# Performance work log

Hardware: AMD Instinct MI355X
Metric: run time of the kernel (lower is better)

The kernel has to match this reference:

```python
import jax, jax.numpy as jnp
import numpy as np

N, E = 30000, 240000          # nodes, edges per view
IN, D, OUT = 512, 128, 64      # in_dim, hidden_dim, out_dim
V, BLK, H, DM = 2, 2, 2, 64    # num_view, blk_size, num_heads, gate max-pool dim
NEG_ATT, NEG_OUT = 0.2, 0.01   # leaky_relu slopes (attention / outer)


def setup_inputs() -> dict:
    key = jax.random.key(0)
    ks = jax.random.split(key, 12)
    s = 0.05
    f32 = jnp.float32
    return {
        "ft": jax.random.normal(ks[0], (N, IN), f32),
        "src": jax.random.randint(ks[1], (V, E), 0, N, jnp.int32),
        "dst": jax.random.randint(ks[2], (V, E), 0, N, jnp.int32),
        "W_proj": jax.random.normal(ks[3], (IN, D), f32) * s,
        "W_embed": jax.random.normal(ks[4], (D, D), f32) * s,
        "a_l": jax.random.normal(ks[5], (V, BLK, H, D), f32) * s,
        "a_r": jax.random.normal(ks[6], (V, BLK, H, D), f32) * s,
        "Wv": jax.random.normal(ks[7], (V, BLK, H, D, D), f32) * s,
        "Wgm": jax.random.normal(ks[8], (V, BLK, D, DM), f32) * s,
        "Wgate": jax.random.normal(ks[9], (V, BLK, 2 * D + DM, H), f32) * s,
        "b_gate": jnp.zeros((V, BLK, H), f32),
        "W_tran": jax.random.normal(ks[10], (2 * D + DM and (D + V * H * D), OUT), f32) * s if False else jax.random.normal(ks[10], (D + V * H * D, OUT), f32) * s,
        "b_tran": jnp.zeros((OUT,), f32),
    }


def _seg_sum(x, idx):
    return jax.ops.segment_sum(x, idx, num_segments=N)


def _cgaan_layer(v, z, s_idx, d_idx, al, ar, wv, wgm, wgate, bg, merge):
    # v: [N,D] values, z: [N,D] attention features ('proj_z')
    # Multi-head attention logits: e_ij = leaky_relu(a_l.z_src + a_r.z_dst)  [E,H]
    logit_l = jnp.einsum("nd,hd->nh", z, al)
    logit_r = jnp.einsum("nd,hd->nh", z, ar)
    e = jax.nn.leaky_relu(logit_l[s_idx] + logit_r[d_idx], NEG_ATT)
    # edge softmax over incoming edges of each dst node
    m = jax.ops.segment_max(e, d_idx, num_segments=N)          # [N,H]
    ex = jnp.exp(e - m[d_idx])
    denom = _seg_sum(ex, d_idx)                                 # [N,H]
    alpha = ex / denom[d_idx]                                   # [E,H]
    # per-head value projection and weighted aggregation
    wvn = jnp.einsum("nd,hde->nhe", v, wv)                      # [N,H,D]
    agg = _seg_sum(alpha[:, :, None] * wvn[s_idx], d_idx)       # [N,H,D]
    # GaAN-style gate: sigmoid(FC([x_i, mean_j v_j, max_j (v_j Wgm)])) -> per-head scalar
    deg = _seg_sum(jnp.ones((s_idx.shape[0],), v.dtype), d_idx)  # [N]
    mean_n = _seg_sum(v[s_idx], d_idx) / jnp.maximum(deg, 1.0)[:, None]
    mx = jax.ops.segment_max((v @ wgm)[s_idx], d_idx, num_segments=N)
    mx = jnp.where(deg[:, None] > 0, mx, 0.0)                   # isolated nodes -> 0
    g = jax.nn.sigmoid(jnp.concatenate([v, mean_n, mx], -1) @ wgate + bg)  # [N,H]
    agg = g[:, :, None] * agg
    if merge == "mean":
        return agg.mean(axis=1)                                 # [N,D]
    return agg.reshape(agg.shape[0], -1)                        # cat -> [N,H*D]


def reference(ft, src, dst, W_proj, W_embed, a_l, a_r, Wv, Wgm, Wgate, b_gate, W_tran, b_tran):
    proj = ft @ W_proj                                          # [N,D]
    cur = [proj for _ in range(V)]
    for i in range(BLK):
        merge = "mean" if i < BLK - 1 else "cat"
        nxt = []
        for j in range(V):
            z = cur[j] @ W_embed
            h = _cgaan_layer(cur[j], z, src[j], dst[j], a_l[j, i], a_r[j, i],
                             Wv[j, i], Wgm[j, i], Wgate[j, i], b_gate[j, i], merge)
            nxt.append(jax.nn.leaky_relu(h, NEG_OUT))
        cur = nxt
    h = jnp.concatenate([proj] + cur, axis=-1)                  # [N, D+V*H*D]
    return h @ W_tran + b_tran
```

## Files before the change

### kernel.cpp

```cpp
#include <hip/hip_runtime.h>
#include <hip/hip_bf16.h>
#include <math.h>

#define NN 30000
#define EE 240000
#define IN_DIM 512
#define DD 128
#define OUTD 64
#define NV 2
#define NBLK 2
#define NH 2
#define DMM 64
#define NEG_ATT 0.2f
#define NEG_OUT 0.01f
#define CH 1024
#define NCH ((NN + CH - 1) / CH)

typedef __attribute__((ext_vector_type(8))) short bf16x8;
typedef __attribute__((ext_vector_type(4))) float f32x4;
typedef __attribute__((ext_vector_type(4))) unsigned short us4;
typedef __attribute__((ext_vector_type(8))) unsigned short us8;

#define OFF_PROJVM 0
#define OFF_WV     131072
#define OFF_WGM    262144
#define OFF_TRAN   278528
#define WT_TOTAL   319488

__device__ __forceinline__ unsigned split_bf(float x) {
  unsigned u = __float_as_uint(x);
  unsigned hb = (u + 0x7FFFu + ((u >> 16) & 1u)) >> 16;
  float hf = __uint_as_float(hb << 16);
  float lo = x - hf;
  unsigned ul = __float_as_uint(lo);
  unsigned lb = (ul + 0x7FFFu + ((ul >> 16) & 1u)) >> 16;
  return hb | (lb << 16);
}

__device__ __forceinline__ unsigned short f2bf(float x) {
  unsigned u = __float_as_uint(x);
  return (unsigned short)((u + 0x7FFFu + ((u >> 16) & 1u)) >> 16);
}
__device__ __forceinline__ float bf2f(unsigned short u) {
  return __uint_as_float((unsigned)u << 16);
}

__device__ __forceinline__ void gload16(void* lds, const void* g) {
  __builtin_amdgcn_global_load_lds((const __attribute__((address_space(1))) unsigned int*)g,
                                   (__attribute__((address_space(3))) unsigned int*)lds, 16, 0, 0);
}

__global__ __launch_bounds__(256) void k_deg(const int* __restrict__ dst, int* __restrict__ deg) {
  int e = blockIdx.x * 256 + threadIdx.x;
  if (e < NV * EE) atomicAdd(&deg[(e / EE) * NN + dst[e]], 1);
}

__global__ __launch_bounds__(256) void k_scan1(const int* __restrict__ deg, int* __restrict__ partial) {
  int b = blockIdx.x, view = b / NCH, ch = b % NCH;
  const int* d = deg + view * NN + ch * CH;
  int rem = min(CH, NN - ch * CH);
  int t = threadIdx.x;
  int s = 0;
  for (int i = t; i < rem; i += 256) s += d[i];
  for (int k = 32; k; k >>= 1) s += __shfl_xor(s, k);
  __shared__ int wsum[4];
  if ((t & 63) == 0) wsum[t >> 6] = s;
  __syncthreads();
  if (t == 0) partial[b] = wsum[0] + wsum[1] + wsum[2] + wsum[3];
}

__global__ void k_scan2(const int* __restrict__ partial, int* __restrict__ chunkoff, int* __restrict__ off) {
  if (threadIdx.x == 0 && blockIdx.x == 0) {
    for (int v = 0; v < NV; v++) {
      int acc = 0;
      for (int c = 0; c < NCH; c++) { chunkoff[v * NCH + c] = acc; acc += partial[v * NCH + c]; }
      off[v * (NN + 1) + NN] = acc;
    }
  }
}

__global__ __launch_bounds__(256) void k_scan3(const int* __restrict__ deg, const int* __restrict__ chunkoff,
                                               int* __restrict__ off) {
  int b = blockIdx.x, view = b / NCH, ch = b % NCH;
  int base = ch * CH;
  const int* d = deg + view * NN;
  int* o = off + view * (NN + 1);
  int t = threadIdx.x, lane = t & 63, w = t >> 6;
  int i0 = base + t * 4;
  int x0 = 0, x1 = 0, x2 = 0, x3 = 0;
  if (i0 + 3 < NN) { int4 q = *(const int4*)(d + i0); x0 = q.x; x1 = q.y; x2 = q.z; x3 = q.w; }
  else {
    if (i0     < NN) x0 = d[i0];
    if (i0 + 1 < NN) x1 = d[i0 + 1];
    if (i0 + 2 < NN) x2 = d[i0 + 2];
  }
  int tot = x0 + x1 + x2 + x3;
  int incl = tot;
  for (int k = 1; k < 64; k <<= 1) { int y = __shfl_up(incl, k); if (lane >= k) incl += y; }
  __shared__ int wt[4];
  if (lane == 63) wt[w] = incl;
  __syncthreads();
  int wexcl = 0;
  for (int k = 0; k < w; k++) wexcl += wt[k];
  int excl = chunkoff[b] + wexcl + incl - tot;
  if (i0     < NN) o[i0]     = excl;
  if (i0 + 1 < NN) o[i0 + 1] = excl + x0;
  if (i0 + 2 < NN) o[i0 + 2] = excl + x0 + x1;
  if (i0 + 3 < NN) o[i0 + 3] = excl + x0 + x1 + x2;
}

__global__ __launch_bounds__(256) void k_fill(const int* __restrict__ src, const int* __restrict__ dst,
                                              const int* __restrict__ off, int* __restrict__ cursor,
                                              int* __restrict__ csr_src) {
  int e = blockIdx.x * 256 + threadIdx.x;
  if (e >= NV * EE) return;
  int view = e / EE;
  int d = dst[e];
  int p = atomicAdd(&cursor[view * NN + d], 1);
  csr_src[view * EE + off[view * (NN + 1) + d] + p] = src[e];
}

__global__ __launch_bounds__(256) void k_prepw(const float* __restrict__ W_embed, const float* __restrict__ a_l,
                                               const float* __restrict__ a_r, const float* __restrict__ Wp,
                                               const float* __restrict__ Wgm,
                                               float* __restrict__ Bl, float* __restrict__ Br,
                                               float* __restrict__ wf) {
  if (blockIdx.x < 256) {
    int idx = blockIdx.x * 256 + threadIdx.x;
    int j = idx >> 15, k = (idx >> 6) & 511, n = idx & 63;
    const float* wp = Wp + (size_t)k * DD;
    const float* wg = Wgm + (size_t)(j * NBLK + 0) * DD * DMM + n;
    float s = 0.f;
    for (int e = 0; e < DD; e++) s += wp[e] * wg[(size_t)e * DMM];
    wf[idx] = s;
  } else {
    int idx = (blockIdx.x - 256) * 256 + threadIdx.x;
    if (idx >= NV * NBLK * DD * NH) return;
    int h = idx & 1, dd = (idx >> 1) & 127, lv = idx >> 8;
    const float* w = W_embed + dd * DD;
    const float* al = a_l + (lv * NH + h) * DD;
    const float* ar = a_r + (lv * NH + h) * DD;
    float sl = 0.f, sr = 0.f;
    for (int e = 0; e < DD; e++) { float we = w[e]; sl += we * al[e]; sr += we * ar[e]; }
    Bl[idx] = sl; Br[idx] = sr;
  }
}

__global__ __launch_bounds__(256) void k_wsplit(const float* __restrict__ Wp, const float* __restrict__ wf,
                                                const float* __restrict__ Wv, const float* __restrict__ Wgm,
                                                const float* __restrict__ Wt,
                                                unsigned short* __restrict__ hi, unsigned short* __restrict__ lo) {
  int y = blockIdx.y;
  const float* src; int K, N; size_t doff;
  if (y == 0)      { src = Wp;                      K = 512; N = 128; doff = OFF_PROJVM; }
  else if (y <= 2) { int j = y - 1; src = wf + (size_t)j * 512 * 64; K = 512; N = 64; doff = OFF_PROJVM + (size_t)(128 + j * 64) * 512; }
  else if (y <= 6) { int lv = y - 3; src = Wv + (size_t)lv * 32768;  K = 256; N = 128; doff = OFF_WV + (size_t)lv * 32768; }
  else if (y <= 8) { int j = y - 7; src = Wgm + (size_t)(j * NBLK + 1) * 8192; K = 128; N = 64; doff = OFF_WGM + (size_t)j * 8192; }
  else             { src = Wt;                      K = 640; N = 64;  doff = OFF_TRAN; }
  int idx = blockIdx.x * 256 + threadIdx.x;
  if (idx >= K * N) return;
  int n = idx / K, k = idx % K;
  int tk = k >> 6, g = (k >> 3) & 7, j2 = k & 7;
  int ks = (tk << 6) | ((g ^ (n & 7)) << 3) | j2;
  unsigned p = split_bf(src[(size_t)k * N + n]);
  hi[doff + (size_t)n * K + ks] = (unsigned short)(p & 0xFFFFu);
  lo[doff + (size_t)n * K + ks] = (unsigned short)(p >> 16);
}

__global__ __launch_bounds__(256) void k_llr(const unsigned short* __restrict__ p0,
                                             const unsigned short* __restrict__ p1, int ps,
                                             const float* __restrict__ Bl0, const float* __restrict__ Br0,
                                             const float* __restrict__ Bl1, const float* __restrict__ Br1,
                                             const float* __restrict__ Wg0, const float* __restrict__ Wg1,
                                             float4* __restrict__ lq, float2* __restrict__ lr) {
  int lane = threadIdx.x & 63, wid = threadIdx.x >> 6;
  int n = blockIdx.x * 4 + wid;
  int k = lane * 2;
  unsigned a = *(const unsigned*)(p0 + (size_t)n * ps + k);
  unsigned b = *(const unsigned*)(p1 + (size_t)n * ps + k);
  float ax = bf2f((unsigned short)a), ay = bf2f((unsigned short)(a >> 16));
  float bx = bf2f((unsigned short)b), by = bf2f((unsigned short)(b >> 16));
  float r[12];
  r[0]  = ax * Bl0[k * 2]     + ay * Bl0[k * 2 + 2];
  r[1]  = ax * Bl0[k * 2 + 1] + ay * Bl0[k * 2 + 3];
  r[2]  = ax * Br0[k * 2]     + ay * Br0[k * 2 + 2];
  r[3]  = ax * Br0[k * 2 + 1] + ay * Br0[k * 2 + 3];
  r[4]  = ax * Wg0[(128 + k) * 2]     + ay * Wg0[(129 + k) * 2];
  r[5]  = ax * Wg0[(128 + k) * 2 + 1] + ay * Wg0[(129 + k) * 2 + 1];
  r[6]  = bx * Bl1[k * 2]     + by * Bl1[k * 2 + 2];
  r[7]  = bx * Bl1[k * 2 + 1] + by * Bl1[k * 2 + 3];
  r[8]  = bx * Br1[k * 2]     + by * Br1[k * 2 + 2];
  r[9]  = bx * Br1[k * 2 + 1] + by * Br1[k * 2 + 3];
  r[10] = bx * Wg1[(128 + k) * 2]     + by * Wg1[(129 + k) * 2];
  r[11] = bx * Wg1[(128 + k) * 2 + 1] + by * Wg1[(129 + k) * 2 + 1];
  for (int s = 32; s; s >>= 1)
#pragma unroll
    for (int q = 0; q < 12; q++) r[q] += __shfl_xor(r[q], s);
  if (lane == 0) {
    lq[n] = make_float4(r[0], r[1], r[4], r[5]);
    lr[n] = make_float2(r[2], r[3]);
    lq[NN + n] = make_float4(r[6], r[7], r[10], r[11]);
    lr[NN + n] = make_float2(r[8], r[9]);
  }
}

__global__ __launch_bounds__(256) void k_edge(const int* __restrict__ off_, const int* __restrict__ csr_,
                                              const float4* __restrict__ lq_, const float2* __restrict__ lr_,
                                              const unsigned short* __restrict__ pk_, long viewStride,
                                              int ps, int vmoff0, int vmstep,
                                              const float* __restrict__ Wg_, const float* __restrict__ bg_,
                                              unsigned short* __restrict__ S_) {
  int view = blockIdx.y;
  const int* off = off_ + view * (NN + 1);
  const int* csr = csr_ + (size_t)view * EE;
  const float4* lq = lq_ + (size_t)view * NN;
  const float2* lrp = lr_ + (size_t)view * NN;
  const unsigned short* pk = pk_ + (size_t)view * viewStride;
  int vmoff = vmoff0 + view * vmstep;
  const float* Wg = Wg_ + (size_t)view * NBLK * (2 * DD + DMM) * NH;
  const float* bg = bg_ + view * NBLK * NH;
  unsigned short* S = S_ + (size_t)view * NN * 256;

  int lane = threadIdx.x & 63, wid = threadIdx.x >> 6;
  int n = blockIdx.x * 4 + wid;
  int e0 = off[n], nb = off[n + 1] - e0;
  int half = lane >> 5, hl = lane & 31;
  if (nb == 0) {
    us4 z4 = {0, 0, 0, 0};
    *(us4*)(S + (size_t)n * 256 + half * 128 + 4 * hl) = z4;
    return;
  }
  float2 lrn = lrp[n];
  float sa0[4] = {0.f, 0.f, 0.f, 0.f}, sa1[4] = {0.f, 0.f, 0.f, 0.f};
  float d0 = 0.f, d1 = 0.f, tm0 = 0.f, tm1 = 0.f, vm0 = -INFINITY, vm1 = -INFINITY;
  for (int base = 0; base < nb; base += 64) {
    int i = base + lane;
    float w0 = 0.f, w1 = 0.f; int sidx = 0;
    if (i < nb) {
      sidx = csr[e0 + i];
      float4 q = lq[sidx];
      float x0 = q.x + lrn.x, x1 = q.y + lrn.y;
      x0 = (x0 > 0.f) ? x0 : NEG_ATT * x0;
      x1 = (x1 > 0.f) ? x1 : NEG_ATT * x1;
      w0 = __expf(x0); w1 = __expf(x1);
      d0 += w0; d1 += w1; tm0 += q.z; tm1 += q.w;
    }
    int cnt = min(64, nb - base);
    for (int s = 0; 2 * s < cnt; s++) {
      int j = 2 * s + half;
      if (j < cnt) {
        int se = __shfl(sidx, j);
        float we0 = __shfl(w0, j), we1 = __shfl(w1, j);
        const unsigned short* rowp = pk + (size_t)se * ps;
        us4 vq = *(const us4*)(rowp + 4 * hl);
        float v0 = bf2f(vq[0]), v1 = bf2f(vq[1]), v2 = bf2f(vq[2]), v3 = bf2f(vq[3]);
        sa0[0] += we0 * v0; sa0[1] += we0 * v1; sa0[2] += we0 * v2; sa0[3] += we0 * v3;
        sa1[0] += we1 * v0; sa1[1] += we1 * v1; sa1[2] += we1 * v2; sa1[3] += we1 * v3;
        unsigned vmu = *(const unsigned*)(rowp + vmoff + 2 * hl);
        vm0 = fmaxf(vm0, bf2f((unsigned short)vmu));
        vm1 = fmaxf(vm1, bf2f((unsigned short)(vmu >> 16)));
      }
    }
  }
#pragma unroll
  for (int k = 0; k < 4; k++) {
    sa0[k] += __shfl_xor(sa0[k], 32);
    sa1[k] += __shfl_xor(sa1[k], 32);
  }
  vm0 = fmaxf(vm0, __shfl_xor(vm0, 32));
  vm1 = fmaxf(vm1, __shfl_xor(vm1, 32));
  for (int s = 32; s; s >>= 1) { d0 += __shfl_xor(d0, s); d1 += __shfl_xor(d1, s); }
  unsigned vnu = *(const unsigned*)(pk + (size_t)n * ps + 2 * lane);
  float vnx = bf2f((unsigned short)vnu), vny = bf2f((unsigned short)(vnu >> 16));
  float im = 1.f / (float)nb;
  float p0 = vnx * Wg[(2 * lane) * 2]     + vny * Wg[(2 * lane + 1) * 2]     + tm0 * im;
  float p1 = vnx * Wg[(2 * lane) * 2 + 1] + vny * Wg[(2 * lane + 1) * 2 + 1] + tm1 * im;
  if (half == 1) {
    p0 += vm0 * Wg[(256 + 2 * hl) * 2]     + vm1 * Wg[(256 + 2 * hl + 1) * 2];
    p1 += vm0 * Wg[(256 + 2 * hl) * 2 + 1] + vm1 * Wg[(256 + 2 * hl + 1) * 2 + 1];
  }
  for (int s = 32; s; s >>= 1) { p0 += __shfl_xor(p0, s); p1 += __shfl_xor(p1, s); }
  float g0 = 1.f / (1.f + __expf(-(p0 + bg[0])));
  float g1 = 1.f / (1.f + __expf(-(p1 + bg[1])));
  float q0 = g0 / d0, q1 = g1 / d1;
  us4 o4;
  if (half == 0) {
    o4[0] = f2bf(sa0[0] * q0); o4[1] = f2bf(sa0[1] * q0);
    o4[2] = f2bf(sa0[2] * q0); o4[3] = f2bf(sa0[3] * q0);
  } else {
    o4[0] = f2bf(sa1[0] * q1); o4[1] = f2bf(sa1[1] * q1);
    o4[2] = f2bf(sa1[2] * q1); o4[3] = f2bf(sa1[3] * q1);
  }
  *(us4*)(S + (size_t)n * 256 + half * 128 + 4 * hl) = o4;
}

struct GB {
  const void* A[4];
  unsigned long long bofs[4];
  float* C[4];
  unsigned short* P[4];
  int ldc[4];
  int pldc[4];
};

template <int BN, bool ABF>
__global__ __launch_bounds__(256) void gemm_mfma(
    GB gb, const unsigned short* __restrict__ Bth, const unsigned short* __restrict__ Btl,
    int lda, int ldb, int M, int K,
    const float* __restrict__ bias, float fs, int flags) {
  constexpr int NSUB = BN / 32;
  constexpr int CPW = BN / 32;
  __shared__ __align__(16) unsigned short Ah[64][64];
  __shared__ __align__(16) unsigned short Al[ABF ? 2 : 64][64];
  __shared__ __align__(16) unsigned short Bh[BN][64], Bl[BN][64];
  int z, xb;
  if (flags & 4) { z = blockIdx.x & 1; xb = blockIdx.x >> 1; }
  else           { z = blockIdx.z;     xb = blockIdx.x; }
  const float* __restrict__ Af = (const float*)gb.A[z];
  const unsigned short* __restrict__ Ab = (const unsigned short*)gb.A[z];
  float* __restrict__ C = gb.C[z];
  unsigned short* __restrict__ P = gb.P[z];
  const int ldc = gb.ldc[z], pldc = gb.pldc[z];
  const size_t bofs = gb.bofs[z];
  const int t = threadIdx.x;
  const int lane = t & 63, wv = t >> 6;
  const int lm = lane & 15, lg = lane >> 4;
  const int m0w = (wv & 1) * 32, n0w = (wv >> 1) * (BN / 2);
  const int row0 = xb * 64;
  f32x4 acc[2][NSUB];
#pragma unroll
  for (int ms = 0; ms < 2; ms++)
#pragma unroll
    for (int ns = 0; ns < NSUB; ns++) acc[ms][ns] = (f32x4)0.f;

  float4 apre[2][2];
  const int ar_ = t >> 3, ag_ = t & 7;

  auto loadA = [&](int k0) {
    if constexpr (!ABF) {
#pragma unroll
      for (int q = 0; q < 2; q++) {
        int rr = row0 + q * 32 + ar_;
        if (rr < M) {
          const float* p = Af + (size_t)rr * lda + k0 + ag_ * 8;
          apre[q][0] = *(const float4*)p;
          apre[q][1] = *(const float4*)(p + 4);
        } else {
          apre[q][0] = make_float4(0.f, 0.f, 0.f, 0.f);
          apre[q][1] = make_float4(0.f, 0.f, 0.f, 0.f);
        }
      }
    }
  };
  auto storeA = [&]() {
    if constexpr (!ABF) {
#pragma unroll
      for (int q = 0; q < 2; q++) {
        int r = q * 32 + ar_;
        us8 h8, l8;
        float vals[8] = {apre[q][0].x, apre[q][0].y, apre[q][0].z, apre[q][0].w,
                         apre[q][1].x, apre[q][1].y, apre[q][1].z, apre[q][1].w};
#pragma unroll
        for (int e = 0; e < 8; e++) {
          unsigned pp = split_bf(vals[e]);
          h8[e] = (unsigned short)(pp & 0xFFFFu);
          l8[e] = (unsigned short)(pp >> 16);
        }
        int c = (ag_ ^ (r & 7)) << 3;
        *(us8*)&Ah[r][c] = h8;
        *(us8*)&Al[r][c] = l8;
      }
    }
  };
  auto stageA_bf = [&](int k0) {
    if constexpr (ABF) {
#pragma unroll
      for (int q = 0; q < 2; q++) {
        int r = q * 32 + ar_;
        int rr = min(row0 + r, M - 1);
        int scg = ag_ ^ (r & 7);
        gload16((char*)&Ah[0][0] + q * 4096 + t * 16,
                Ab + (size_t)rr * lda + k0 + scg * 8);
      }
    }
  };
  auto stageB = [&](int k0) {
#pragma unroll
    for (int q = 0; q < CPW; q++) {
      int chunk = wv * CPW + q;
      int o = chunk * 1024 + lane * 16;
      int n = o >> 7;
      int pq = (o >> 4) & 7;
      size_t gofs = bofs + (size_t)n * ldb + k0 + pq * 8;
      gload16((char*)&Bh[0][0] + o, Bth + gofs);
      gload16((char*)&Bl[0][0] + o, Btl + gofs);
    }
  };

  loadA(0);
  for (int k0 = 0; k0 < K; k0 += 64) {
    if constexpr (ABF) stageA_bf(k0); else storeA();
    stageB(k0);
    __syncthreads();
    if constexpr (!ABF) { if (k0 + 64 < K) loadA(k0 + 64); }
#pragma unroll
    for (int kc = 0; kc < 2; kc++) {
      bf16x8 afh[2], afl[2], bfh[NSUB], bfl[NSUB];
#pragma unroll
      for (int ms = 0; ms < 2; ms++) {
        int R = m0w + ms * 16 + lm;
        int c = (((kc * 4 + lg) ^ (R & 7)) << 3);
        afh[ms] = *(const bf16x8*)&Ah[R][c];
        if constexpr (!ABF) afl[ms] = *(const bf16x8*)&Al[R][c];
      }
#pragma unroll
      for (int ns = 0; ns < NSUB; ns++) {
        int R = n0w + ns * 16 + lm;
        int c = (((kc * 4 + lg) ^ (R & 7)) << 3);
        bfh[ns] = *(const bf16x8*)&Bh[R][c];
        bfl[ns] = *(const bf16x8*)&Bl[R][c];
      }
#pragma unroll
      for (int ms = 0; ms < 2; ms++)
#pragma unroll
        for (int ns = 0; ns < NSUB; ns++) {
          if constexpr (!ABF)
            acc[ms][ns] = __builtin_amdgcn_mfma_f32_16x16x32_bf16(afl[ms], bfh[ns], acc[ms][ns], 0, 0, 0);
          acc[ms][ns] = __builtin_amdgcn_mfma_f32_16x16x32_bf16(afh[ms], bfl[ns], acc[ms][ns], 0, 0, 0);
          acc[ms][ns] = __builtin_amdgcn_mfma_f32_16x16x32_bf16(afh[ms], bfh[ns], acc[ms][ns], 0, 0, 0);
        }
    }
    __syncthreads();
  }
#pragma unroll
  for (int ms = 0; ms < 2; ms++)
#pragma unroll
    for (int ns = 0; ns < NSUB; ns++)
#pragma unroll
      for (int j = 0; j < 4; j++) {
        int row = row0 + m0w + ms * 16 + lg * 4 + j;
        if (row >= M) continue;
        int col = n0w + ns * 16 + lm;
        float val = acc[ms][ns][j] * fs;
        if (bias) val += bias[col];
        if (flags & 2) val = (val > 0.f) ? val : NEG_OUT * val;
        if (C) C[(size_t)row * ldc + col] = val;
        if (P) P[(size_t)row * pldc + col] = f2bf(val);
      }
}

extern "C" void kernel_launch(void* const* d_in, const int* in_sizes, int n_in,
                              void* d_out, int out_size, void* d_ws, size_t ws_size,
                              hipStream_t stream) {
  const float* ft      = (const float*)d_in[0];
  const int*   src     = (const int*)  d_in[1];
  const int*   dst     = (const int*)  d_in[2];
  const float* W_proj  = (const float*)d_in[3];
  const float* W_embed = (const float*)d_in[4];
  const float* a_l     = (const float*)d_in[5];
  const float* a_r     = (const float*)d_in[6];
  const float* Wv      = (const float*)d_in[7];
  const float* Wgm     = (const float*)d_in[8];
  const float* Wgate   = (const float*)d_in[9];
  const float* b_gate  = (const float*)d_in[10];
  const float* W_tran  = (const float*)d_in[11];
  const float* b_tran  = (const float*)d_in[12];
  float* out = (float*)d_out;
  char* ws = (char*)d_ws;
  (void)in_sizes; (void)n_in; (void)out_size; (void)ws_size;

  size_t o = 0;
  auto take = [&](size_t bytes) { size_t r = o; o += (bytes + 255) & ~(size_t)255; return r; };
  int*   deg     = (int*)(ws + take((size_t)NV * NN * 4));
  int*   cursor  = (int*)(ws + take((size_t)NV * NN * 4));
  int*   csr_off = (int*)(ws + take((size_t)NV * (NN + 1) * 4));
  int*   csr_src = (int*)(ws + take((size_t)NV * EE * 4));
  int*   partial = (int*)(ws + take((size_t)NV * NCH * 4));
  int*   chunkoff= (int*)(ws + take((size_t)NV * NCH * 4));
  float* Bl      = (float*)(ws + take((size_t)NV * NBLK * DD * NH * 4));
  float* Br      = (float*)(ws + take((size_t)NV * NBLK * DD * NH * 4));
  float* wf      = (float*)(ws + take((size_t)NV * 512 * 64 * 4));
  unsigned short* whi = (unsigned short*)(ws + take((size_t)WT_TOTAL * 2));
  unsigned short* wlo = (unsigned short*)(ws + take((size_t)WT_TOTAL * 2));
  float* h       = (float*)(ws + take((size_t)NN * 640 * 4));
  unsigned short* pk0 = (unsigned short*)(ws + take((size_t)NN * 256 * 2));
  unsigned short* pk1 = (unsigned short*)(ws + take((size_t)NV * NN * 192 * 2));
  unsigned short* Sbf = (unsigned short*)(ws + take((size_t)NV * NN * 256 * 2));
  float4* lqb    = (float4*)(ws + take((size_t)NV * NN * 16));
  float2* lrb    = (float2*)(ws + take((size_t)NV * NN * 8));

  const int HSTR = 640;

  hipMemsetAsync(deg, 0, (size_t)(((size_t)NV * NN * 4 + 255) & ~(size_t)255) + (size_t)NV * NN * 4, stream);
  k_deg<<<(NV * EE + 255) / 256, 256, 0, stream>>>(dst, deg);
  k_scan1<<<NV * NCH, 256, 0, stream>>>(deg, partial);
  k_scan2<<<1, 64, 0, stream>>>(partial, chunkoff, csr_off);
  k_scan3<<<NV * NCH, 256, 0, stream>>>(deg, chunkoff, csr_off);
  k_fill<<<(NV * EE + 255) / 256, 256, 0, stream>>>(src, dst, csr_off, cursor, csr_src);
  k_prepw<<<260, 256, 0, stream>>>(W_embed, a_l, a_r, W_proj, Wgm, Bl, Br, wf);
  k_wsplit<<<dim3(256, 10), 256, 0, stream>>>(W_proj, wf, Wv, Wgm, W_tran, whi, wlo);

  const int GM = (NN + 63) / 64;

  {
    GB gb = {};
    gb.A[0] = ft; gb.A[1] = ft;
    gb.bofs[0] = OFF_PROJVM; gb.bofs[1] = OFF_PROJVM + (size_t)128 * 512;
    gb.C[0] = h;  gb.ldc[0] = HSTR;
    gb.P[0] = pk0;       gb.pldc[0] = 256;
    gb.P[1] = pk0 + 128; gb.pldc[1] = 256;
    gemm_mfma<128, false><<<dim3(GM * 2, 1, 1), 256, 0, stream>>>(gb, whi, wlo, IN_DIM, 512, NN, 512,
                                                                  nullptr, 1.f, 4);
  }

  k_llr<<<NN / 4, 256, 0, stream>>>(pk0, pk0, 256,
                                    Bl + 0 * 256, Br + 0 * 256, Bl + 2 * 256, Br + 2 * 256,
                                    Wgate, Wgate + (size_t)NBLK * 320 * NH,
                                    lqb, lrb);
  k_edge<<<dim3(NN / 4, 2), 256, 0, stream>>>(csr_off, csr_src, lqb, lrb,
                                              pk0, 0L, 256, 128, 64,
                                              Wgate, b_gate, Sbf);
  {
    GB gb = {};
    for (int j = 0; j < 2; j++) {
      gb.A[j] = Sbf + (size_t)j * NN * 256;
      gb.bofs[j] = OFF_WV + (size_t)(j * 2) * 32768;
      gb.P[j] = pk1 + (size_t)j * NN * 192;
      gb.pldc[j] = 192;
    }
    gemm_mfma<128, true><<<dim3(GM, 1, 2), 256, 0, stream>>>(gb, whi, wlo, 256, 256, NN, 256,
                                                             nullptr, 0.5f, 2);
  }
  {
    GB gb = {};
    for (int j = 0; j < 2; j++) {
      gb.A[j] = pk1 + (size_t)j * NN * 192;
      gb.bofs[j] = OFF_WGM + (size_t)j * 8192;
      gb.P[j] = pk1 + (size_t)j * NN * 192 + 128;
      gb.pldc[j] = 192;
    }
    gemm_mfma<64, true><<<dim3(GM, 1, 2), 256, 0, stream>>>(gb, whi, wlo, 192, 128, NN, 128,
                                                            nullptr, 1.f, 0);
  }
  k_llr<<<NN / 4, 256, 0, stream>>>(pk1, pk1 + (size_t)NN * 192, 192,
                                    Bl + 1 * 256, Br + 1 * 256, Bl + 3 * 256, Br + 3 * 256,
                                    Wgate + 640, Wgate + (size_t)NBLK * 640 + 640,
                                    lqb, lrb);
  k_edge<<<dim3(NN / 4, 2), 256, 0, stream>>>(csr_off, csr_src, lqb, lrb,
                                              pk1, (long)NN * 192, 192, 128, 0,
                                              Wgate + 640, b_gate + NH, Sbf);
  {
    GB gb = {};
    for (int z = 0; z < 4; z++) {
      int j = z >> 1, hd = z & 1;
      gb.A[z] = Sbf + (size_t)j * NN * 256 + hd * 128;
      gb.bofs[z] = OFF_WV + (size_t)(j * 2 + 1) * 32768 + hd * 128;
      gb.C[z] = h + 128 + z * 128;
      gb.ldc[z] = HSTR;
    }
    gemm_mfma<128, true><<<dim3(GM, 1, 4), 256, 0, stream>>>(gb, whi, wlo, 256, 256, NN, 128,
                                                             nullptr, 1.f, 2);
  }
  {
    GB gb = {};
    gb.A[0] = h; gb.bofs[0] = OFF_TRAN; gb.C[0] = out; gb.ldc[0] = OUTD;
    gemm_mfma<64, false><<<dim3(GM, 1, 1), 256, 0, stream>>>(gb, whi, wlo, HSTR, 640, NN, 640,
                                                             b_tran, 1.f, 0);
  }
}
```

Baseline: 334.7 us.

## Merge setup kernels, widen edge gather, drop A-low split in GEMM

Fuses the degree count with weight preparation, and the first scan pass with weight splitting, so the setup phase needs fewer launches. The edge aggregation kernel now processes four edges per iteration with 8-wide bf16 loads per lane instead of two edges with 4-wide loads. The fp32-input GEMM no longer computes a low-bf16 residual of A, which drops one MFMA per tile and the Al LDS buffer at the cost of accuracy. The z-interleaved block mapping flag is replaced by blockIdx.z.

Result: slower. 341.6 us (+2.1%).

```diff
diff --git a/kernel.cpp b/kernel.cpp
--- a/kernel.cpp
+++ b/kernel.cpp
@@ -36,7 +36,6 @@
   unsigned lb = (ul + 0x7FFFu + ((ul >> 16) & 1u)) >> 16;
   return hb | (lb << 16);
 }
-
 __device__ __forceinline__ unsigned short f2bf(float x) {
   unsigned u = __float_as_uint(x);
   return (unsigned short)((u + 0x7FFFu + ((u >> 16) & 1u)) >> 16);
@@ -44,29 +43,85 @@
 __device__ __forceinline__ float bf2f(unsigned short u) {
   return __uint_as_float((unsigned)u << 16);
 }
-
 __device__ __forceinline__ void gload16(void* lds, const void* g) {
   __builtin_amdgcn_global_load_lds((const __attribute__((address_space(1))) unsigned int*)g,
                                    (__attribute__((address_space(3))) unsigned int*)lds, 16, 0, 0);
 }
 
-__global__ __launch_bounds__(256) void k_deg(const int* __restrict__ dst, int* __restrict__ deg) {
-  int e = blockIdx.x * 256 + threadIdx.x;
-  if (e < NV * EE) atomicAdd(&deg[(e / EE) * NN + dst[e]], 1);
-}
-
-__global__ __launch_bounds__(256) void k_scan1(const int* __restrict__ deg, int* __restrict__ partial) {
-  int b = blockIdx.x, view = b / NCH, ch = b % NCH;
-  const int* d = deg + view * NN + ch * CH;
-  int rem = min(CH, NN - ch * CH);
-  int t = threadIdx.x;
-  int s = 0;
-  for (int i = t; i < rem; i += 256) s += d[i];
-  for (int k = 32; k; k >>= 1) s += __shfl_xor(s, k);
-  __shared__ int wsum[4];
-  if ((t & 63) == 0) wsum[t >> 6] = s;
-  __syncthreads();
-  if (t == 0) partial[b] = wsum[0] + wsum[1] + wsum[2] + wsum[3];
+__global__ __launch_bounds__(256) void kA_deg_prepw(const int* __restrict__ dst, int* __restrict__ deg,
+                                                    const float* __restrict__ W_embed,
+                                                    const float* __restrict__ a_l, const float* __restrict__ a_r,
+                                                    const float* __restrict__ Wp, const float* __restrict__ Wgm,
+                                                    float* __restrict__ Bl, float* __restrict__ Br,
+                                                    float* __restrict__ wf) {
+  int b = blockIdx.x;
+  if (b < 1875) {
+    int e = b * 256 + threadIdx.x;
+    if (e < NV * EE) atomicAdd(&deg[(e / EE) * NN + dst[e]], 1);
+    return;
+  }
+  int pb = b - 1875;
+  if (pb < 256) {
+    int idx = pb * 256 + threadIdx.x;
+    int j = idx >> 15, k = (idx >> 6) & 511, n = idx & 63;
+    const float* wp = Wp + (size_t)k * DD;
+    const float* wg = Wgm + (size_t)(j * NBLK + 0) * DD * DMM + n;
+    float s = 0.f;
+    for (int e = 0; e < DD; e++) s += wp[e] * wg[(size_t)e * DMM];
+    wf[idx] = s;
+  } else {
+    int idx = (pb - 256) * 256 + threadIdx.x;
+    if (idx >= NV * NBLK * DD * NH) return;
+    int h = idx & 1, dd = (idx >> 1) & 127, lv = idx >> 8;
+    const float* w = W_embed + dd * DD;
+    const float* al = a_l + (lv * NH + h) * DD;
+    const float* ar = a_r + (lv * NH + h) * DD;
+    float sl = 0.f, sr = 0.f;
+    for (int e = 0; e < DD; e++) { float we = w[e]; sl += we * al[e]; sr += we * ar[e]; }
+    Bl[idx] = sl; Br[idx] = sr;
+  }
+}
+
+__global__ __launch_bounds__(256) void kB_scan1_wsplit(const int* __restrict__ deg, int* __restrict__ partial,
+                                                       const float* __restrict__ Wp, const float* __restrict__ wf,
+                                                       const float* __restrict__ Wv, const float* __restrict__ Wgm,
+                                                       const float* __restrict__ Wt,
+                                                       unsigned short* __restrict__ hi,
+                                                       unsigned short* __restrict__ lo) {
+  int b = blockIdx.x;
+  if (b < 60) {
+    int view = b / NCH, ch = b % NCH;
+    const int* d = deg + view * NN + ch * CH;
+    int rem = min(CH, NN - ch * CH);
+    int t = threadIdx.x;
+    int s = 0;
+    for (int i = t; i < rem; i += 256) s += d[i];
+    for (int k = 32; k; k >>= 1) s += __shfl_xor(s, k);
+    __shared__ int wsum[4];
+    if ((t & 63) == 0) wsum[t >> 6] = s;
+    __syncthreads();
+    if (t == 0) partial[b] = wsum[0] + wsum[1] + wsum[2] + wsum[3];
+    return;
+  }
+  int wb = b - 60;
+  const int pre[11] = {0, 256, 384, 512, 640, 768, 896, 1024, 1056, 1088, 1248};
+  int y = 0;
+  while (y < 10 && wb >= pre[y + 1]) y++;
+  int bx = wb - pre[y];
+  const float* src; int K, N; size_t doff;
+  if (y == 0)      { src = Wp;                      K = 512; N = 128; doff = OFF_PROJVM; }
+  else if (y <= 2) { int j = y - 1; src = wf + (size_t)j * 512 * 64; K = 512; N = 64; doff = OFF_PROJVM + (size_t)(128 + j * 64) * 512; }
+  else if (y <= 6) { int lv = y - 3; src = Wv + (size_t)lv * 32768;  K = 256; N = 128; doff = OFF_WV + (size_t)lv * 32768; }
+  else if (y <= 8) { int j = y - 7; src = Wgm + (size_t)(j * NBLK + 1) * 8192; K = 128; N = 64; doff = OFF_WGM + (size_t)j * 8192; }
+  else             { src = Wt;                      K = 640; N = 64;  doff = OFF_TRAN; }
+  int idx = bx * 256 + threadIdx.x;
+  if (idx >= K * N) return;
+  int n = idx / K, k = idx % K;
+  int tk = k >> 6, g = (k >> 3) & 7, j2 = k & 7;
+  int ks = (tk << 6) | ((g ^ (n & 7)) << 3) | j2;
+  unsigned p = split_bf(src[(size_t)k * N + n]);
+  hi[doff + (size_t)n * K + ks] = (unsigned short)(p & 0xFFFFu);
+  lo[doff + (size_t)n * K + ks] = (unsigned short)(p >> 16);
 }
 
 __global__ void k_scan2(const int* __restrict__ partial, int* __restrict__ chunkoff, int* __restrict__ off) {
@@ -118,53 +173,6 @@
   int d = dst[e];
   int p = atomicAdd(&cursor[view * NN + d], 1);
   csr_src[view * EE + off[view * (NN + 1) + d] + p] = src[e];
-}
-
-__global__ __launch_bounds__(256) void k_prepw(const float* __restrict__ W_embed, const float* __restrict__ a_l,
-                                               const float* __restrict__ a_r, const float* __restrict__ Wp,
-                                               const float* __restrict__ Wgm,
-                                               float* __restrict__ Bl, float* __restrict__ Br,
-                                               float* __restrict__ wf) {
-  if (blockIdx.x < 256) {
-    int idx = blockIdx.x * 256 + threadIdx.x;
-    int j = idx >> 15, k = (idx >> 6) & 511, n = idx & 63;
-    const float* wp = Wp + (size_t)k * DD;
-    const float* wg = Wgm + (size_t)(j * NBLK + 0) * DD * DMM + n;
-    float s = 0.f;
-    for (int e = 0; e < DD; e++) s += wp[e] * wg[(size_t)e * DMM];
-    wf[idx] = s;
-  } else {
-    int idx = (blockIdx.x - 256) * 256 + threadIdx.x;
-    if (idx >= NV * NBLK * DD * NH) return;
-    int h = idx & 1, dd = (idx >> 1) & 127, lv = idx >> 8;
-    const float* w = W_embed + dd * DD;
-    const float* al = a_l + (lv * NH + h) * DD;
-    const float* ar = a_r + (lv * NH + h) * DD;
-    float sl = 0.f, sr = 0.f;
-    for (int e = 0; e < DD; e++) { float we = w[e]; sl += we * al[e]; sr += we * ar[e]; }
-    Bl[idx] = sl; Br[idx] = sr;
-  }
-}
-
-__global__ __launch_bounds__(256) void k_wsplit(const float* __restrict__ Wp, const float* __restrict__ wf,
-                                                const float* __restrict__ Wv, const float* __restrict__ Wgm,
-                                                const float* __restrict__ Wt,
-                                                unsigned short* __restrict__ hi, unsigned short* __restrict__ lo) {
-  int y = blockIdx.y;
-  const float* src; int K, N; size_t doff;
-  if (y == 0)      { src = Wp;                      K = 512; N = 128; doff = OFF_PROJVM; }
-  else if (y <= 2) { int j = y - 1; src = wf + (size_t)j * 512 * 64; K = 512; N = 64; doff = OFF_PROJVM + (size_t)(128 + j * 64) * 512; }
-  else if (y <= 6) { int lv = y - 3; src = Wv + (size_t)lv * 32768;  K = 256; N = 128; doff = OFF_WV + (size_t)lv * 32768; }
-  else if (y <= 8) { int j = y - 7; src = Wgm + (size_t)(j * NBLK + 1) * 8192; K = 128; N = 64; doff = OFF_WGM + (size_t)j * 8192; }
-  else             { src = Wt;                      K = 640; N = 64;  doff = OFF_TRAN; }
-  int idx = blockIdx.x * 256 + threadIdx.x;
-  if (idx >= K * N) return;
-  int n = idx / K, k = idx % K;
-  int tk = k >> 6, g = (k >> 3) & 7, j2 = k & 7;
-  int ks = (tk << 6) | ((g ^ (n & 7)) << 3) | j2;
-  unsigned p = split_bf(src[(size_t)k * N + n]);
-  hi[doff + (size_t)n * K + ks] = (unsigned short)(p & 0xFFFFu);
-  lo[doff + (size_t)n * K + ks] = (unsigned short)(p >> 16);
 }
 
 __global__ __launch_bounds__(256) void k_llr(const unsigned short* __restrict__ p0,
@@ -224,74 +232,85 @@
   int lane = threadIdx.x & 63, wid = threadIdx.x >> 6;
   int n = blockIdx.x * 4 + wid;
   int e0 = off[n], nb = off[n + 1] - e0;
-  int half = lane >> 5, hl = lane & 31;
+  int q4 = lane >> 4, l16 = lane & 15;
   if (nb == 0) {
-    us4 z4 = {0, 0, 0, 0};
-    *(us4*)(S + (size_t)n * 256 + half * 128 + 4 * hl) = z4;
+    if (lane < 32) {
+      us8 z8 = {0, 0, 0, 0, 0, 0, 0, 0};
+      *(us8*)(S + (size_t)n * 256 + q4 * 128 + l16 * 8) = z8;
+    }
     return;
   }
   float2 lrn = lrp[n];
-  float sa0[4] = {0.f, 0.f, 0.f, 0.f}, sa1[4] = {0.f, 0.f, 0.f, 0.f};
-  float d0 = 0.f, d1 = 0.f, tm0 = 0.f, tm1 = 0.f, vm0 = -INFINITY, vm1 = -INFINITY;
+  float sa0[8] = {0.f}, sa1[8] = {0.f};
+  float vmm[4] = {-INFINITY, -INFINITY, -INFINITY, -INFINITY};
+  float d0 = 0.f, d1 = 0.f, tm0 = 0.f, tm1 = 0.f;
   for (int base = 0; base < nb; base += 64) {
     int i = base + lane;
     float w0 = 0.f, w1 = 0.f; int sidx = 0;
     if (i < nb) {
       sidx = csr[e0 + i];
-      float4 q = lq[sidx];
-      float x0 = q.x + lrn.x, x1 = q.y + lrn.y;
+      float4 qq = lq[sidx];
+      float x0 = qq.x + lrn.x, x1 = qq.y + lrn.y;
       x0 = (x0 > 0.f) ? x0 : NEG_ATT * x0;
       x1 = (x1 > 0.f) ? x1 : NEG_ATT * x1;
       w0 = __expf(x0); w1 = __expf(x1);
-      d0 += w0; d1 += w1; tm0 += q.z; tm1 += q.w;
+      d0 += w0; d1 += w1; tm0 += qq.z; tm1 += qq.w;
     }
     int cnt = min(64, nb - base);
-    for (int s = 0; 2 * s < cnt; s++) {
-      int j = 2 * s + half;
+    for (int s = 0; 4 * s < cnt; s++) {
+      int j = 4 * s + q4;
       if (j < cnt) {
         int se = __shfl(sidx, j);
         float we0 = __shfl(w0, j), we1 = __shfl(w1, j);
         const unsigned short* rowp = pk + (size_t)se * ps;
-        us4 vq = *(const us4*)(rowp + 4 * hl);
-        float v0 = bf2f(vq[0]), v1 = bf2f(vq[1]), v2 = bf2f(vq[2]), v3 = bf2f(vq[3]);
-        sa0[0] += we0 * v0; sa0[1] += we0 * v1; sa0[2] += we0 * v2; sa0[3] += we0 * v3;
-        sa1[0] += we1 * v0; sa1[1] += we1 * v1; sa1[2] += we1 * v2; sa1[3] += we1 * v3;
-        unsigned vmu = *(const unsigned*)(rowp + vmoff + 2 * hl);
-        vm0 = fmaxf(vm0, bf2f((unsigned short)vmu));
-        vm1 = fmaxf(vm1, bf2f((unsigned short)(vmu >> 16)));
-      }
-    }
+        us8 vq = *(const us8*)(rowp + l16 * 8);
+#pragma unroll
+        for (int k = 0; k < 8; k++) {
+          float v = bf2f(vq[k]);
+          sa0[k] += we0 * v; sa1[k] += we1 * v;
+        }
+        us4 vmq = *(const us4*)(rowp + vmoff + l16 * 4);
+#pragma unroll
+        for (int k = 0; k < 4; k++) vmm[k] = fmaxf(vmm[k], bf2f(vmq[k]));
+      }
+    }
+  }
+#pragma unroll
+  for (int k = 0; k < 8; k++) {
+    sa0[k] += __shfl_xor(sa0[k], 16); sa0[k] += __shfl_xor(sa0[k], 32);
+    sa1[k] += __shfl_xor(sa1[k], 16); sa1[k] += __shfl_xor(sa1[k], 32);
   }
 #pragma unroll
   for (int k = 0; k < 4; k++) {
-    sa0[k] += __shfl_xor(sa0[k], 32);
-    sa1[k] += __shfl_xor(sa1[k], 32);
-  }
-  vm0 = fmaxf(vm0, __shfl_xor(vm0, 32));
-  vm1 = fmaxf(vm1, __shfl_xor(vm1, 32));
+    vmm[k] = fmaxf(vmm[k], __shfl_xor(vmm[k], 16));
+    vmm[k] = fmaxf(vmm[k], __shfl_xor(vmm[k], 32));
+  }
   for (int s = 32; s; s >>= 1) { d0 += __shfl_xor(d0, s); d1 += __shfl_xor(d1, s); }
   unsigned vnu = *(const unsigned*)(pk + (size_t)n * ps + 2 * lane);
   float vnx = bf2f((unsigned short)vnu), vny = bf2f((unsigned short)(vnu >> 16));
   float im = 1.f / (float)nb;
   float p0 = vnx * Wg[(2 * lane) * 2]     + vny * Wg[(2 * lane + 1) * 2]     + tm0 * im;
   float p1 = vnx * Wg[(2 * lane) * 2 + 1] + vny * Wg[(2 * lane + 1) * 2 + 1] + tm1 * im;
-  if (half == 1) {
-    p0 += vm0 * Wg[(256 + 2 * hl) * 2]     + vm1 * Wg[(256 + 2 * hl + 1) * 2];
-    p1 += vm0 * Wg[(256 + 2 * hl) * 2 + 1] + vm1 * Wg[(256 + 2 * hl + 1) * 2 + 1];
+  if (q4 == 1) {
+#pragma unroll
+    for (int k = 0; k < 4; k++) {
+      int d = l16 * 4 + k;
+      p0 += vmm[k] * Wg[(256 + d) * 2];
+      p1 += vmm[k] * Wg[(256 + d) * 2 + 1];
+    }
   }
   for (int s = 32; s; s >>= 1) { p0 += __shfl_xor(p0, s); p1 += __shfl_xor(p1, s); }
   float g0 = 1.f / (1.f + __expf(-(p0 + bg[0])));
   float g1 = 1.f / (1.f + __expf(-(p1 + bg[1])));
   float q0 = g0 / d0, q1 = g1 / d1;
-  us4 o4;
-  if (half == 0) {
-    o4[0] = f2bf(sa0[0] * q0); o4[1] = f2bf(sa0[1] * q0);
-    o4[2] = f2bf(sa0[2] * q0); o4[3] = f2bf(sa0[3] * q0);
-  } else {
-    o4[0] = f2bf(sa1[0] * q1); o4[1] = f2bf(sa1[1] * q1);
-    o4[2] = f2bf(sa1[2] * q1); o4[3] = f2bf(sa1[3] * q1);
-  }
-  *(us4*)(S + (size_t)n * 256 + half * 128 + 4 * hl) = o4;
+  if (lane < 32) {
+    const float* sp = q4 ? sa1 : sa0;
+    float qq = q4 ? q1 : q0;
+    us8 o8;
+#pragma unroll
+    for (int k = 0; k < 8; k++) o8[k] = f2bf(sp[k] * qq);
+    *(us8*)(S + (size_t)n * 256 + q4 * 128 + l16 * 8) = o8;
+  }
 }
 
 struct GB {
@@ -311,11 +330,8 @@
   constexpr int NSUB = BN / 32;
   constexpr int CPW = BN / 32;
   __shared__ __align__(16) unsigned short Ah[64][64];
-  __shared__ __align__(16) unsigned short Al[ABF ? 2 : 64][64];
   __shared__ __align__(16) unsigned short Bh[BN][64], Bl[BN][64];
-  int z, xb;
-  if (flags & 4) { z = blockIdx.x & 1; xb = blockIdx.x >> 1; }
-  else           { z = blockIdx.z;     xb = blockIdx.x; }
+  const int z = blockIdx.z, xb = blockIdx.x;
   const float* __restrict__ Af = (const float*)gb.A[z];
   const unsigned short* __restrict__ Ab = (const unsigned short*)gb.A[z];
   float* __restrict__ C = gb.C[z];
@@ -357,18 +373,13 @@
 #pragma unroll
       for (int q = 0; q < 2; q++) {
         int r = q * 32 + ar_;
-        us8 h8, l8;
+        us8 h8;
         float vals[8] = {apre[q][0].x, apre[q][0].y, apre[q][0].z, apre[q][0].w,
                          apre[q][1].x, apre[q][1].y, apre[q][1].z, apre[q][1].w};
 #pragma unroll
-        for (int e = 0; e < 8; e++) {
-          unsigned pp = split_bf(vals[e]);
-          h8[e] = (unsigned short)(pp & 0xFFFFu);
-          l8[e] = (unsigned short)(pp >> 16);
-        }
+        for (int e = 0; e < 8; e++) h8[e] = f2bf(vals[e]);
         int c = (ag_ ^ (r & 7)) << 3;
         *(us8*)&Ah[r][c] = h8;
-        *(us8*)&Al[r][c] = l8;
       }
     }
   };
@@ -405,13 +416,12 @@
     if constexpr (!ABF) { if (k0 + 64 < K) loadA(k0 + 64); }
 #pragma unroll
     for (int kc = 0; kc < 2; kc++) {
-      bf16x8 afh[2], afl[2], bfh[NSUB], bfl[NSUB];
+      bf16x8 afh[2], bfh[NSUB], bfl[NSUB];
 #pragma unroll
       for (int ms = 0; ms < 2; ms++) {
         int R = m0w + ms * 16 + lm;
         int c = (((kc * 4 + lg) ^ (R & 7)) << 3);
         afh[ms] = *(const bf16x8*)&Ah[R][c];
-        if constexpr (!ABF) afl[ms] = *(const bf16x8*)&Al[R][c];
       }
 #pragma unroll
       for (int ns = 0; ns < NSUB; ns++) {
@@ -424,8 +434,6 @@
       for (int ms = 0; ms < 2; ms++)
 #pragma unroll
         for (int ns = 0; ns < NSUB; ns++) {
-          if constexpr (!ABF)
-            acc[ms][ns] = __builtin_amdgcn_mfma_f32_16x16x32_bf16(afl[ms], bfh[ns], acc[ms][ns], 0, 0, 0);
           acc[ms][ns] = __builtin_amdgcn_mfma_f32_16x16x32_bf16(afh[ms], bfl[ns], acc[ms][ns], 0, 0, 0);
           acc[ms][ns] = __builtin_amdgcn_mfma_f32_16x16x32_bf16(afh[ms], bfh[ns], acc[ms][ns], 0, 0, 0);
         }
@@ -492,13 +500,11 @@
   const int HSTR = 640;
 
   hipMemsetAsync(deg, 0, (size_t)(((size_t)NV * NN * 4 + 255) & ~(size_t)255) + (size_t)NV * NN * 4, stream);
-  k_deg<<<(NV * EE + 255) / 256, 256, 0, stream>>>(dst, deg);
-  k_scan1<<<NV * NCH, 256, 0, stream>>>(deg, partial);
+  kA_deg_prepw<<<2135, 256, 0, stream>>>(dst, deg, W_embed, a_l, a_r, W_proj, Wgm, Bl, Br, wf);
+  kB_scan1_wsplit<<<1308, 256, 0, stream>>>(deg, partial, W_proj, wf, Wv, Wgm, W_tran, whi, wlo);
   k_scan2<<<1, 64, 0, stream>>>(partial, chunkoff, csr_off);
   k_scan3<<<NV * NCH, 256, 0, stream>>>(deg, chunkoff, csr_off);
   k_fill<<<(NV * EE + 255) / 256, 256, 0, stream>>>(src, dst, csr_off, cursor, csr_src);
-  k_prepw<<<260, 256, 0, stream>>>(W_embed, a_l, a_r, W_proj, Wgm, Bl, Br, wf);
-  k_wsplit<<<dim3(256, 10), 256, 0, stream>>>(W_proj, wf, Wv, Wgm, W_tran, whi, wlo);
 
   const int GM = (NN + 63) / 64;
 
@@ -509,8 +515,8 @@
     gb.C[0] = h;  gb.ldc[0] = HSTR;
     gb.P[0] = pk0;       gb.pldc[0] = 256;
     gb.P[1] = pk0 + 128; gb.pldc[1] = 256;
-    gemm_mfma<128, false><<<dim3(GM * 2, 1, 1), 256, 0, stream>>>(gb, whi, wlo, IN_DIM, 512, NN, 512,
-                                                                  nullptr, 1.f, 4);
+    gemm_mfma<128, false><<<dim3(GM, 1, 2), 256, 0, stream>>>(gb, whi, wlo, IN_DIM, 512, NN, 512,
+                                                              nullptr, 1.f, 0);
   }
 
   k_llr<<<NN / 4, 256, 0, stream>>>(pk0, pk0, 256,
```
